# Performance work log

Hardware: AMD Instinct MI355X
Metric: run time of the kernel (lower is better)

The kernel has to match this reference:

```python
import jax, jax.numpy as jnp
import numpy as np

B, S, H, M = 8, 4096, 1024, 1024
TEMP = 1.0


def setup_inputs() -> dict:
    key = jax.random.key(0)
    ks = jax.random.split(key, 6)
    sd = 1.0 / np.sqrt(H)
    return {
        "hidden_states": jax.random.normal(ks[0], (B, S, H), jnp.float32),
        "Wq": jax.random.normal(ks[1], (H, H), jnp.float32) * sd,
        "bq": jnp.zeros((H,), jnp.float32),
        "Wk": jax.random.normal(ks[2], (H, H), jnp.float32) * sd,
        "bk": jnp.zeros((H,), jnp.float32),
        "Wv": jax.random.normal(ks[3], (H, H), jnp.float32) * sd,
        "bv": jnp.zeros((H,), jnp.float32),
        "Wo": jax.random.normal(ks[4], (H, 2 * H), jnp.float32) * (1.0 / np.sqrt(2 * H)),
        "bo": jnp.zeros((H,), jnp.float32),
    }


def _l2_normalize(x, eps=1e-12):
    # matches F.normalize(p=2, dim=-1): x / max(||x||, eps)
    n = jnp.sqrt(jnp.sum(x * x, axis=-1, keepdims=True))
    return x / jnp.maximum(n, eps)


def reference(hidden_states, Wq, bq, Wk, bk, Wv, bv, Wo, bo):
    b, s, h = hidden_states.shape
    # _initialize_memory: evenly sample M positions along seq (seq_len >= memory_size)
    idx = jnp.linspace(0.0, s - 1, M).astype(jnp.int32)
    init_states = hidden_states[:, idx]                 # [B, M, H]
    memory_keys = init_states @ Wk.T + bk               # [B, M, H]
    memory_values = init_states @ Wv.T + bv             # [B, M, H]

    query_keys = hidden_states @ Wq.T + bq              # [B, S, H]
    qn = _l2_normalize(query_keys)
    kn = _l2_normalize(memory_keys)
    sim = jnp.einsum('bsh,bmh->bsm', qn, kn) / TEMP     # cosine similarity
    attn = jax.nn.softmax(sim, axis=-1)                 # [B, S, M]
    retrieved = jnp.einsum('bsm,bmh->bsh', attn, memory_values)

    combined = jnp.concatenate([hidden_states, retrieved], axis=-1)  # [B, S, 2H]
    enhanced = combined @ Wo.T + bo                     # [B, S, H]
    return enhanced
```

## Files before the change

kernel.cpp:

```cpp
#include <hip/hip_runtime.h>
#include <hip/hip_bf16.h>
#include <type_traits>
#include <stdint.h>

#define AS1 __attribute__((address_space(1)))
#define AS3 __attribute__((address_space(3)))

typedef __attribute__((ext_vector_type(8))) short short8;
typedef __attribute__((ext_vector_type(4))) short short4v;
typedef __attribute__((ext_vector_type(4))) float floatx4;

#define B_DIM 8
#define S_DIM 4096
#define H_DIM 1024
#define M_DIM 1024

__device__ __forceinline__ float b2f(short s) {
  union { unsigned u; float f; } x;
  x.u = ((unsigned)(unsigned short)s) << 16;
  return x.f;
}
__device__ __forceinline__ short f2b(float f) {
  union { float f; unsigned u; } x;
  x.f = f;
  unsigned u = x.u;
  unsigned r = (u + 0x7fffu + ((u >> 16) & 1u)) >> 16;
  return (short)(unsigned short)r;
}

#define SCHEDB() __builtin_amdgcn_sched_barrier(0)
#define VMCNT(N) asm volatile("s_waitcnt vmcnt(" #N ")")
#define BARRIER() do { SCHEDB(); __builtin_amdgcn_s_barrier(); SCHEDB(); } while (0)

__device__ __forceinline__ void async16(const void* g, void* l) {
  __builtin_amdgcn_global_load_lds((const AS1 void*)g, (AS3 void*)l, 16, 0, 0);
}

__global__ __launch_bounds__(256) void k_cvt(const float4* __restrict__ in,
                                             short4v* __restrict__ out, int n4) {
  const int stride = gridDim.x * 256;
  for (int i = blockIdx.x * 256 + threadIdx.x; i < n4; i += stride) {
    float4 v = in[i];
    short4v o = { f2b(v.x), f2b(v.y), f2b(v.z), f2b(v.w) };
    out[i] = o;
  }
}

__global__ __launch_bounds__(256) void k_cvtw(const float4* __restrict__ Wq,
                                              const float4* __restrict__ Wk,
                                              const float4* __restrict__ Wv,
                                              const float4* __restrict__ Wo,
                                              short4v* __restrict__ wq,
                                              short4v* __restrict__ wk,
                                              short4v* __restrict__ wv,
                                              short4v* __restrict__ wo) {
  const int stride = gridDim.x * 256;
  for (int i = blockIdx.x * 256 + threadIdx.x; i < 1310720; i += stride) {
    const float4* src; short4v* dst; int j;
    if (i < 262144)      { src = Wq; dst = wq; j = i; }
    else if (i < 524288) { src = Wk; dst = wk; j = i - 262144; }
    else if (i < 786432) { src = Wv; dst = wv; j = i - 524288; }
    else                 { src = Wo; dst = wo; j = i - 786432; }
    float4 v = src[j];
    short4v o = { f2b(v.x), f2b(v.y), f2b(v.z), f2b(v.w) };
    dst[j] = o;
  }
}

template<int AMODE, int EPI, bool HAS_BIAS, typename OutT>
__global__ __launch_bounds__(512, 2)
void k_gemm256(const short* __restrict__ A, const short* __restrict__ A2,
               const short* __restrict__ Bw,
               const float* __restrict__ bias, const float* __restrict__ bias2,
               OutT* __restrict__ C, short* __restrict__ Cv,
               int K, long sA, long sB, long sC)
{
  __shared__ __align__(16) short lds[2][2][256 * 64];

  const int t512 = threadIdx.x;
  const int l = t512 & 63;
  const int w = t512 >> 6;
  const int wm = w >> 2, wn = w & 3;
  const int z = blockIdx.z;

  const int gx = gridDim.x, gy = gridDim.y;
  const int orig = blockIdx.y * gx + blockIdx.x;
  const int nwg = gx * gy;
  int s = orig;
  if ((nwg & 7) == 0) {
    const int q8 = nwg >> 3;
    s = (orig & 7) * q8 + (orig >> 3);
  }
  const int row0 = (s / gy) * 256;
  const int col0 = (s % gy) * 256;

  const short* Az = A + (size_t)z * sA;
  const short* Bz = Bw + (size_t)z * sB;

  const int rloc = t512 >> 3;
  const int slot = t512 & 7;
  const int sw = slot ^ (rloc & 7);
  const int nt = K >> 6;

  const int lr = l & 15;
  const int lkb = (l >> 4) << 4;
  const int aswz = (lr & 7) << 4;
  const int aRowByte = (wm * 128 + lr) * 128;
  const int bRowByte = (wn * 64 + lr) * 128;

  auto srcA = [&](int R, int tile) -> const char* {
    if constexpr (AMODE == 2) {
      const size_t row = (size_t)(row0 + R + rloc);
      if (tile < 16) return (const char*)A  + ((row * 1024 + (size_t)tile * 64) << 1) + (sw << 4);
      else           return (const char*)A2 + ((row * 1024 + (size_t)(tile - 16) * 64) << 1) + (sw << 4);
    } else if constexpr (AMODE == 1) {
      const int r = row0 + R + rloc;
      const unsigned m = (unsigned)(r & (M_DIM - 1));
      const int g = (r >> 10) * S_DIM + (int)((m * 4095u) / 1023u);
      return (const char*)A + (((size_t)g * H_DIM + (size_t)tile * 64) << 1) + (sw << 4);
    } else {
      return (const char*)Az + (((size_t)(row0 + R + rloc) * K + (size_t)tile * 64) << 1) + (sw << 4);
    }
  };
  auto srcB = [&](int R, int tile) -> const char* {
    return (const char*)Bz + (((size_t)(col0 + R + rloc) * K + (size_t)tile * 64) << 1) + (sw << 4);
  };
  auto SA = [&](int buf, int R, int tile) {
    async16(srcA(R, tile), (char*)&lds[buf][0][0] + (size_t)(R + w * 8) * 128);
  };
  auto SB = [&](int buf, int R, int tile) {
    async16(srcB(R, tile), (char*)&lds[buf][1][0] + (size_t)(R + w * 8) * 128);
  };

  floatx4 acc[8][4];
  #pragma unroll
  for (int i = 0; i < 8; ++i)
    #pragma unroll
    for (int j = 0; j < 4; ++j)
      acc[i][j] = (floatx4){0.f, 0.f, 0.f, 0.f};

  {
    const int t1 = (nt > 1) ? 1 : 0;
    SA(0, 0, 0);  SA(0, 64, 0); SA(0, 128, 0); SA(0, 192, 0);
    SB(0, 0, 0);  SB(0, 64, 0); SB(0, 128, 0); SB(0, 192, 0);
    SA(1, 0, t1); SA(1, 128, t1);
    SB(1, 0, t1); SB(1, 64, t1); SB(1, 128, t1); SB(1, 192, t1);
    SCHEDB();
    VMCNT(6);
    BARRIER();
  }

#define RD_A4(dst, ldsbase, Mh, ks)                                               \
  {                                                                               \
    _Pragma("unroll")                                                             \
    for (int mi = 0; mi < 4; ++mi)                                                \
      dst[mi] = *(const short8*)((ldsbase) + aRowByte + (Mh) * 8192 +             \
                                 mi * 2048 + ((((ks) * 64) + lkb) ^ aswz));       \
  }
#define RD_B4(dst, ldsbase, ks)                                                   \
  {                                                                               \
    _Pragma("unroll")                                                             \
    for (int ni = 0; ni < 4; ++ni)                                                \
      dst[ni] = *(const short8*)((ldsbase) + bRowByte + ni * 2048 +               \
                                 ((((ks) * 64) + lkb) ^ aswz));                   \
  }
#define MFMA16(Mh, av, bv)                                                        \
  {                                                                               \
    __builtin_amdgcn_s_setprio(1);                                                \
    _Pragma("unroll")                                                             \
    for (int mi = 0; mi < 4; ++mi)                                                \
      _Pragma("unroll")                                                           \
      for (int ni = 0; ni < 4; ++ni)                                              \
        acc[(Mh) * 4 + mi][ni] = __builtin_amdgcn_mfma_f32_16x16x32_bf16(         \
            av[mi], bv[ni], acc[(Mh) * 4 + mi][ni], 0, 0, 0);                     \
    __builtin_amdgcn_s_setprio(0);                                                \
  }

  short8 afX[4], afY[4], bf0[4], bf1[4];

  {
    const char* L0A = (const char*)&lds[0][0][0];
    const char* L0B = (const char*)&lds[0][1][0];
    RD_A4(afX, L0A, 0, 0);
    RD_B4(bf0, L0B, 0);
  }

  for (int t = 0; t < nt; ++t) {
    const int b = t & 1;
    const char* LA  = (const char*)&lds[b][0][0];
    const char* LB  = (const char*)&lds[b][1][0];
    const char* LA1 = (const char*)&lds[b ^ 1][0][0];
    const char* LB1 = (const char*)&lds[b ^ 1][1][0];
    const int tn  = (t + 1 < nt) ? t + 1 : nt - 1;
    const int tn2 = (t + 2 < nt) ? t + 2 : nt - 1;

    RD_A4(afY, LA, 1, 0);
    SA(b ^ 1, 64, tn); SA(b ^ 1, 192, tn);
    BARRIER();
    MFMA16(0, afX, bf0);
    BARRIER();

    RD_A4(afX, LA, 0, 1);
    RD_B4(bf1, LB, 1);
    BARRIER();
    MFMA16(1, afY, bf0);
    BARRIER();

    RD_A4(afY, LA, 1, 1);
    BARRIER();
    MFMA16(0, afX, bf1);
    SCHEDB();
    VMCNT(2);
    BARRIER();

    RD_A4(afX, LA1, 0, 0);
    RD_B4(bf0, LB1, 0);
    SA(b, 0, tn2); SA(b, 128, tn2);
    SB(b, 0, tn2); SB(b, 64, tn2); SB(b, 128, tn2); SB(b, 192, tn2);
    BARRIER();
    MFMA16(1, afY, bf1);
    SCHEDB();
    VMCNT(6);
    BARRIER();
  }
#undef RD_A4
#undef RD_B4
#undef MFMA16

  SCHEDB();
  VMCNT(0);
  SCHEDB();

  OutT* Cz = C + (size_t)z * sC;
  const int rsub = (l >> 4) * 4;
  #pragma unroll
  for (int ni = 0; ni < 4; ++ni) {
    const int colg = col0 + wn * 64 + ni * 16 + lr;
    float bvv = 0.f;
    if constexpr (HAS_BIAS) {
      if constexpr (EPI == 1) bvv = (colg < 1024) ? bias[colg] : bias2[colg - 1024];
      else bvv = bias[colg];
    }
    #pragma unroll
    for (int m = 0; m < 8; ++m) {
      const int rg = row0 + wm * 128 + (m >> 2) * 64 + (m & 3) * 16 + rsub;
      #pragma unroll
      for (int j = 0; j < 4; ++j) {
        const float v = acc[m][ni][j] + bvv;
        const int rr = rg + j;
        if constexpr (EPI == 1) {
          if (colg < 1024) {
            ((short*)C)[(size_t)rr * 1024 + colg] = f2b(v);
          } else {
            const int bb = rr >> 10, mm = rr & (M_DIM - 1);
            Cv[((size_t)bb * H_DIM + (colg - 1024)) * M_DIM + mm] = f2b(v);
          }
        } else {
          const size_t o = (size_t)rr * 1024 + colg;
          if constexpr (std::is_same<OutT, float>::value) Cz[o] = v;
          else Cz[o] = f2b(v);
        }
      }
    }
  }
}

__global__ __launch_bounds__(256) void k_rownorm(const short* __restrict__ x,
                                                 float* __restrict__ inv) {
  const int w = threadIdx.x >> 6, l = threadIdx.x & 63;
  const size_t row = (size_t)blockIdx.x * 4 + w;
  const short* p = x + row * 1024 + l * 16;
  short8 v0 = *(const short8*)p;
  short8 v1 = *(const short8*)(p + 8);
  float ss = 0.f;
  #pragma unroll
  for (int i = 0; i < 8; ++i) {
    const float a = b2f(v0[i]), b = b2f(v1[i]);
    ss += a * a + b * b;
  }
  #pragma unroll
  for (int o = 32; o > 0; o >>= 1) ss += __shfl_xor(ss, o, 64);
  if (l == 0) inv[row] = 1.f / fmaxf(sqrtf(ss), 1e-12f);
}

__global__ __launch_bounds__(256) void k_softmax(short* __restrict__ sbuf,
                                                 const float* __restrict__ qinv,
                                                 const float* __restrict__ kinv) {
  const int w = threadIdx.x >> 6, l = threadIdx.x & 63;
  const size_t row = (size_t)blockIdx.x * 4 + w;
  short* p = sbuf + row * 1024 + l * 16;
  const float qi = qinv[row];
  const float* kv = kinv + ((row >> 12) << 10) + l * 16;
  float ki[16];
  *(float4*)&ki[0]  = *(const float4*)(kv);
  *(float4*)&ki[4]  = *(const float4*)(kv + 4);
  *(float4*)&ki[8]  = *(const float4*)(kv + 8);
  *(float4*)&ki[12] = *(const float4*)(kv + 12);
  short8 v0 = *(short8*)p;
  short8 v1 = *(short8*)(p + 8);
  float f[16];
  #pragma unroll
  for (int i = 0; i < 8; ++i) {
    f[i]     = b2f(v0[i]) * qi * ki[i];
    f[8 + i] = b2f(v1[i]) * qi * ki[8 + i];
  }
  float mx = f[0];
  #pragma unroll
  for (int i = 1; i < 16; ++i) mx = fmaxf(mx, f[i]);
  #pragma unroll
  for (int o = 32; o > 0; o >>= 1) mx = fmaxf(mx, __shfl_xor(mx, o, 64));
  float s = 0.f;
  #pragma unroll
  for (int i = 0; i < 16; ++i) { f[i] = __expf(f[i] - mx); s += f[i]; }
  #pragma unroll
  for (int o = 32; o > 0; o >>= 1) s += __shfl_xor(s, o, 64);
  const float inv = 1.f / s;
  #pragma unroll
  for (int i = 0; i < 8; ++i) { v0[i] = f2b(f[i] * inv); v1[i] = f2b(f[8 + i] * inv); }
  *(short8*)p = v0;
  *(short8*)(p + 8) = v1;
}

extern "C" void kernel_launch(void* const* d_in, const int* in_sizes, int n_in,
                              void* d_out, int out_size, void* d_ws, size_t ws_size,
                              hipStream_t stream)
{
  const float* hid = (const float*)d_in[0];
  const float* Wq  = (const float*)d_in[1];
  const float* bq  = (const float*)d_in[2];
  const float* Wk  = (const float*)d_in[3];
  const float* bk  = (const float*)d_in[4];
  const float* Wv  = (const float*)d_in[5];
  const float* bv  = (const float*)d_in[6];
  const float* Wo  = (const float*)d_in[7];
  const float* bo  = (const float*)d_in[8];

  char* ws = (char*)d_ws;
  short* hb  = (short*)(ws);
  short* qb  = (short*)(ws + (size_t)67108864);
  short* knb = (short*)(ws + (size_t)134217728);
  short* mvT = (short*)(ws + (size_t)150994944);
  short* wqb = (short*)(ws + (size_t)167772160);
  short* wkb = (short*)(ws + (size_t)169869312);
  short* wvb = (short*)(ws + (size_t)171966464);
  short* wob = (short*)(ws + (size_t)174063616);
  short* sb  = (short*)d_out;
  float* qinv = (float*)((char*)d_out + (size_t)67108864);
  float* kinv = (float*)((char*)d_out + (size_t)67108864 + 131072);
  short* rb  = qb;
  float* out = (float*)d_out;

  k_cvt<<<4096, 256, 0, stream>>>((const float4*)hid, (short4v*)hb, 33554432 / 4);
  k_cvtw<<<1280, 256, 0, stream>>>((const float4*)Wq, (const float4*)Wk,
                                   (const float4*)Wv, (const float4*)Wo,
                                   (short4v*)wqb, (short4v*)wkb, (short4v*)wvb, (short4v*)wob);

  k_gemm256<0, 0, true, short><<<dim3(128, 4, 1), 512, 0, stream>>>(
      hb, nullptr, wqb, bq, nullptr, qb, nullptr, 1024, 0, 0, 0);
  k_gemm256<1, 1, true, short><<<dim3(32, 8, 1), 512, 0, stream>>>(
      hb, nullptr, wkb, bk, bv, knb, mvT, 1024, 0, 0, 0);
  k_rownorm<<<8192, 256, 0, stream>>>(qb, qinv);
  k_rownorm<<<2048, 256, 0, stream>>>(knb, kinv);
  k_gemm256<0, 0, false, short><<<dim3(16, 4, 8), 512, 0, stream>>>(
      qb, nullptr, knb, nullptr, nullptr, sb, nullptr, 1024,
      (long)S_DIM * H_DIM, (long)M_DIM * H_DIM, (long)S_DIM * M_DIM);
  k_softmax<<<8192, 256, 0, stream>>>(sb, qinv, kinv);
  k_gemm256<0, 0, false, short><<<dim3(16, 4, 8), 512, 0, stream>>>(
      sb, nullptr, mvT, nullptr, nullptr, rb, nullptr, 1024,
      (long)S_DIM * M_DIM, (long)H_DIM * M_DIM, (long)S_DIM * H_DIM);
  k_gemm256<2, 0, true, float><<<dim3(128, 4, 1), 512, 0, stream>>>(
      hb, rb, wob, bo, nullptr, out, nullptr, 2048, 0, 0, 0);
}
```

Before: 523.2 us.

## Fold value projection into output weights to drop the retrieved-state GEMM

New measurement: 469.6 us, median of 2. 1.11x faster.

```diff
diff --git a/kernel.cpp b/kernel.cpp
--- a/kernel.cpp
+++ b/kernel.cpp
@@ -70,10 +70,10 @@
 template<int AMODE, int EPI, bool HAS_BIAS, typename OutT>
 __global__ __launch_bounds__(512, 2)
 void k_gemm256(const short* __restrict__ A, const short* __restrict__ A2,
-               const short* __restrict__ Bw,
+               const short* __restrict__ Bw, const short* __restrict__ B2,
                const float* __restrict__ bias, const float* __restrict__ bias2,
                OutT* __restrict__ C, short* __restrict__ Cv,
-               int K, long sA, long sB, long sC)
+               int K, long lda, long ldb, long sA, long sB, long sC)
 {
   __shared__ __align__(16) short lds[2][2][256 * 64];
 
@@ -109,7 +109,7 @@
   const int bRowByte = (wn * 64 + lr) * 128;
 
   auto srcA = [&](int R, int tile) -> const char* {
-    if constexpr (AMODE == 2) {
+    if constexpr (AMODE == 2 || AMODE == 3) {
       const size_t row = (size_t)(row0 + R + rloc);
       if (tile < 16) return (const char*)A  + ((row * 1024 + (size_t)tile * 64) << 1) + (sw << 4);
       else           return (const char*)A2 + ((row * 1024 + (size_t)(tile - 16) * 64) << 1) + (sw << 4);
@@ -119,11 +119,18 @@
       const int g = (r >> 10) * S_DIM + (int)((m * 4095u) / 1023u);
       return (const char*)A + (((size_t)g * H_DIM + (size_t)tile * 64) << 1) + (sw << 4);
     } else {
-      return (const char*)Az + (((size_t)(row0 + R + rloc) * K + (size_t)tile * 64) << 1) + (sw << 4);
+      return (const char*)Az + (((size_t)(row0 + R + rloc) * lda + (size_t)tile * 64) << 1) + (sw << 4);
     }
   };
   auto srcB = [&](int R, int tile) -> const char* {
-    return (const char*)Bz + (((size_t)(col0 + R + rloc) * K + (size_t)tile * 64) << 1) + (sw << 4);
+    if constexpr (AMODE == 3) {
+      const size_t row = (size_t)(col0 + R + rloc);
+      if (tile < 16) return (const char*)Bw + ((row * ldb + (size_t)tile * 64) << 1) + (sw << 4);
+      else           return (const char*)B2 + (((size_t)(row0 >> 12) * 1048576 +
+                                                row * 1024 + (size_t)(tile - 16) * 64) << 1) + (sw << 4);
+    } else {
+      return (const char*)Bz + (((size_t)(col0 + R + rloc) * ldb + (size_t)tile * 64) << 1) + (sw << 4);
+    }
   };
   auto SA = [&](int buf, int R, int tile) {
     async16(srcA(R, tile), (char*)&lds[buf][0][0] + (size_t)(R + w * 8) * 128);
@@ -249,12 +256,8 @@
         const float v = acc[m][ni][j] + bvv;
         const int rr = rg + j;
         if constexpr (EPI == 1) {
-          if (colg < 1024) {
-            ((short*)C)[(size_t)rr * 1024 + colg] = f2b(v);
-          } else {
-            const int bb = rr >> 10, mm = rr & (M_DIM - 1);
-            Cv[((size_t)bb * H_DIM + (colg - 1024)) * M_DIM + mm] = f2b(v);
-          }
+          if (colg < 1024) ((short*)C)[(size_t)rr * 1024 + colg] = f2b(v);
+          else             Cv[(size_t)rr * 1024 + (colg - 1024)] = f2b(v);
         } else {
           const size_t o = (size_t)rr * 1024 + colg;
           if constexpr (std::is_same<OutT, float>::value) Cz[o] = v;
@@ -283,12 +286,14 @@
   if (l == 0) inv[row] = 1.f / fmaxf(sqrtf(ss), 1e-12f);
 }
 
-__global__ __launch_bounds__(256) void k_softmax(short* __restrict__ sbuf,
+__global__ __launch_bounds__(256) void k_softmax(const short* __restrict__ sbuf,
+                                                 short* __restrict__ abuf,
                                                  const float* __restrict__ qinv,
                                                  const float* __restrict__ kinv) {
   const int w = threadIdx.x >> 6, l = threadIdx.x & 63;
   const size_t row = (size_t)blockIdx.x * 4 + w;
-  short* p = sbuf + row * 1024 + l * 16;
+  const short* p = sbuf + row * 1024 + l * 16;
+  short* po = abuf + row * 1024 + l * 16;
   const float qi = qinv[row];
   const float* kv = kinv + ((row >> 12) << 10) + l * 16;
   float ki[16];
@@ -296,8 +301,8 @@
   *(float4*)&ki[4]  = *(const float4*)(kv + 4);
   *(float4*)&ki[8]  = *(const float4*)(kv + 8);
   *(float4*)&ki[12] = *(const float4*)(kv + 12);
-  short8 v0 = *(short8*)p;
-  short8 v1 = *(short8*)(p + 8);
+  short8 v0 = *(const short8*)p;
+  short8 v1 = *(const short8*)(p + 8);
   float f[16];
   #pragma unroll
   for (int i = 0; i < 8; ++i) {
@@ -317,8 +322,8 @@
   const float inv = 1.f / s;
   #pragma unroll
   for (int i = 0; i < 8; ++i) { v0[i] = f2b(f[i] * inv); v1[i] = f2b(f[8 + i] * inv); }
-  *(short8*)p = v0;
-  *(short8*)(p + 8) = v1;
+  *(short8*)po = v0;
+  *(short8*)(po + 8) = v1;
 }
 
 extern "C" void kernel_launch(void* const* d_in, const int* in_sizes, int n_in,
@@ -339,15 +344,16 @@
   short* hb  = (short*)(ws);
   short* qb  = (short*)(ws + (size_t)67108864);
   short* knb = (short*)(ws + (size_t)134217728);
-  short* mvT = (short*)(ws + (size_t)150994944);
+  short* mvb = (short*)(ws + (size_t)150994944);
   short* wqb = (short*)(ws + (size_t)167772160);
   short* wkb = (short*)(ws + (size_t)169869312);
   short* wvb = (short*)(ws + (size_t)171966464);
   short* wob = (short*)(ws + (size_t)174063616);
+  short* ab  = qb;
+  short* vwt = knb;
   short* sb  = (short*)d_out;
   float* qinv = (float*)((char*)d_out + (size_t)67108864);
   float* kinv = (float*)((char*)d_out + (size_t)67108864 + 131072);
-  short* rb  = qb;
   float* out = (float*)d_out;
 
   k_cvt<<<4096, 256, 0, stream>>>((const float4*)hid, (short4v*)hb, 33554432 / 4);
@@ -356,18 +362,21 @@
                                    (short4v*)wqb, (short4v*)wkb, (short4v*)wvb, (short4v*)wob);
 
   k_gemm256<0, 0, true, short><<<dim3(128, 4, 1), 512, 0, stream>>>(
-      hb, nullptr, wqb, bq, nullptr, qb, nullptr, 1024, 0, 0, 0);
+      hb, nullptr, wqb, nullptr, bq, nullptr, qb, nullptr,
+      1024, 1024, 1024, 0, 0, 0);
   k_gemm256<1, 1, true, short><<<dim3(32, 8, 1), 512, 0, stream>>>(
-      hb, nullptr, wkb, bk, bv, knb, mvT, 1024, 0, 0, 0);
+      hb, nullptr, wkb, nullptr, bk, bv, knb, mvb,
+      1024, 1024, 1024, 0, 0, 0);
   k_rownorm<<<8192, 256, 0, stream>>>(qb, qinv);
   k_rownorm<<<2048, 256, 0, stream>>>(knb, kinv);
   k_gemm256<0, 0, false, short><<<dim3(16, 4, 8), 512, 0, stream>>>(
-      qb, nullptr, knb, nullptr, nullptr, sb, nullptr, 1024,
-      (long)S_DIM * H_DIM, (long)M_DIM * H_DIM, (long)S_DIM * M_DIM);
-  k_softmax<<<8192, 256, 0, stream>>>(sb, qinv, kinv);
-  k_gemm256<0, 0, false, short><<<dim3(16, 4, 8), 512, 0, stream>>>(
-      sb, nullptr, mvT, nullptr, nullptr, rb, nullptr, 1024,
-      (long)S_DIM * M_DIM, (long)H_DIM * M_DIM, (long)S_DIM * H_DIM);
-  k_gemm256<2, 0, true, float><<<dim3(128, 4, 1), 512, 0, stream>>>(
-      hb, rb, wob, bo, nullptr, out, nullptr, 2048, 0, 0, 0);
-}
+      qb, nullptr, knb, nullptr, nullptr, nullptr, sb, nullptr,
+      1024, 1024, 1024, (long)S_DIM * H_DIM, (long)M_DIM * H_DIM, (long)S_DIM * M_DIM);
+  k_gemm256<0, 0, false, short><<<dim3(4, 4, 8), 512, 0, stream>>>(
+      wob + 1024, nullptr, mvb, nullptr, nullptr, nullptr, vwt, nullptr,
+      1024, 2048, 1024, 0, (long)M_DIM * H_DIM, (long)M_DIM * H_DIM);
+  k_softmax<<<8192, 256, 0, stream>>>(sb, ab, qinv, kinv);
+  k_gemm256<3, 0, true, float><<<dim3(128, 4, 1), 512, 0, stream>>>(
+      hb, ab, wob, vwt, bo, nullptr, out, nullptr,
+      2048, 1024, 2048, 0, 0, 0);
+}
```
